# Kernel tuning notes

Hardware: AMD Instinct MI355X
Metric: run time of the kernel (lower is better)

The kernel has to match this reference:

```python
import jax, jax.numpy as jnp
import numpy as np

NE, NR = 100000, 50
E, H, M = 512, 8, 8
HD = E // H
B = 65536


def setup_inputs() -> dict:
    key = jax.random.key(0)
    ks = jax.random.split(key, 24)
    xav = lambda k, shp: jax.random.normal(k, shp, jnp.float32) * (2.0 / (shp[0] + shp[-1])) ** 0.5
    return {
        'entity_emb': xav(ks[0], (NE, E)),
        'relation_emb': xav(ks[1], (NR, E)),
        'dens_ent_emb': jax.random.normal(ks[2], (NE, E), jnp.float32) * 0.02,
        'dens_ent_w': xav(ks[3], (E, 1)), 'dens_ent_b': jnp.zeros((1,), jnp.float32),
        'dens_rel_emb': jax.random.normal(ks[4], (NR, E), jnp.float32) * 0.02,
        'dens_rel_w': xav(ks[5], (E, 1)), 'dens_rel_b': jnp.zeros((1,), jnp.float32),
        'local_motifs': xav(ks[6], (M, HD)),
        'global_motifs': xav(ks[7], (M, HD)),
        'Wq': xav(ks[8], (E, E)), 'bq': jnp.zeros((E,), jnp.float32),
        'Wkl': xav(ks[9], (HD, HD)), 'bkl': jnp.zeros((HD,), jnp.float32),
        'Wkg': xav(ks[10], (HD, HD)), 'bkg': jnp.zeros((HD,), jnp.float32),
        'Wout': xav(ks[11], (2 * E, E)), 'bout': jnp.zeros((E,), jnp.float32),
        'adv_w': jnp.float32(1.0), 'adv_b': jnp.float32(0.0),
        'h_idx': jax.random.randint(ks[12], (B,), 0, NE),
        'r_idx': jax.random.randint(ks[13], (B,), 0, NR),
        't_idx': jax.random.randint(ks[14], (B,), 0, NE),
    }


def reference(entity_emb, relation_emb, dens_ent_emb, dens_ent_w, dens_ent_b,
              dens_rel_emb, dens_rel_w, dens_rel_b, local_motifs, global_motifs,
              Wq, bq, Wkl, bkl, Wkg, bkg, Wout, bout, adv_w, adv_b,
              h_idx, r_idx, t_idx):
    h = entity_emb[h_idx]           # [B, E]
    r = relation_emb[r_idx]
    t = entity_emb[t_idx]
    # density gating: sigmoid(Linear(Embedding(idx))) per head/tail/relation, averaged
    h_d = jax.nn.sigmoid(dens_ent_emb[h_idx] @ dens_ent_w + dens_ent_b)   # [B,1]
    t_d = jax.nn.sigmoid(dens_ent_emb[t_idx] @ dens_ent_w + dens_ent_b)
    r_d = jax.nn.sigmoid(dens_rel_emb[r_idx] @ dens_rel_w + dens_rel_b)
    density = (h_d + t_d + r_d) / 3.0                                     # [B,1]
    diff = h + r - t
    # hierarchical soft attention over local/global motif codebooks
    ctx = h + r + t
    q = (ctx @ Wq + bq).reshape(-1, H, HD)                                # [B,H,HD]
    lk = local_motifs @ Wkl + bkl                                         # [M,HD]
    gk = global_motifs @ Wkg + bkg
    scale = 1.0 / jnp.sqrt(jnp.asarray(HD, q.dtype))
    dens = density[:, :, None]                                            # [B,1,1]
    l_w = jax.nn.softmax(jnp.einsum('bhd,md->bhm', q, lk) * scale + dens, axis=-1)
    g_w = jax.nn.softmax(jnp.einsum('bhd,md->bhm', q, gk) * scale + dens, axis=-1)
    attn = (l_w + g_w) / 2.0                                              # [B,H,M]
    motifs = local_motifs + global_motifs                                 # [M,HD]
    motif_repr = jnp.einsum('bhm,md->bhd', attn, motifs).reshape(-1, E)   # [B,E]
    motif_loss = jnp.sum((diff - motif_repr) ** 2, axis=-1)               # ||.||^2
    combined = jnp.concatenate([diff, motif_repr], axis=-1)               # [B,2E]
    transformed = jnp.tanh(combined @ Wout + bout)
    score = adv_w * jnp.linalg.norm(transformed, axis=-1) + adv_b
    return score, motif_loss
```

## Files before the change

kernel.cpp:

```cpp
#include <hip/hip_runtime.h>
#include <math.h>

#define B_TOT 65536

typedef __attribute__((ext_vector_type(4))) float f32x4;
typedef __attribute__((ext_vector_type(4))) unsigned int u32x4;
typedef __attribute__((ext_vector_type(8))) __bf16 bf16x8;

#define OFF_WLOGT 0u
#define OFF_CBIAS 131072u
#define OFF_BCAT  131584u
#define OFF_MOTIF 721408u
#define OFF_LK    723456u
#define OFF_GK    725504u
#define OFF_G     727552u
#define OFF_DIFF  1048576u
#define OFF_ATTN  68157440u
#define OFF_SSQ   76546048u

__device__ __forceinline__ unsigned short f2bf(float x) {
  union { float f; unsigned int u; } v; v.f = x;
  return (unsigned short)((v.u + 0x7FFFu + ((v.u >> 16) & 1u)) >> 16);
}

__device__ __forceinline__ float bf2f(unsigned short u) {
  union { unsigned int i; float f; } v; v.i = ((unsigned int)u) << 16; return v.f;
}

__device__ __forceinline__ float fast_tanh(float x) {
  float cx = fminf(fmaxf(x, -15.f), 15.f);
  float e = __expf(2.f * cx);
  return 1.f - 2.f * __builtin_amdgcn_rcpf(e + 1.f);
}

__global__ __launch_bounds__(256) void k0a(
    const float* __restrict__ lm, const float* __restrict__ gm,
    const float* __restrict__ Wkl, const float* __restrict__ bkl,
    const float* __restrict__ Wkg, const float* __restrict__ bkg,
    const float* __restrict__ bq,
    float* __restrict__ lk, float* __restrict__ gk,
    float* __restrict__ motifs, float* __restrict__ G, float* __restrict__ cb) {
  int tid = threadIdx.x;
  for (int o = tid; o < 512; o += 256) {
    int m = o >> 6, d = o & 63;
    float s1 = bkl[d], s2 = bkg[d];
    for (int k = 0; k < 64; ++k) {
      s1 += lm[m*64+k] * Wkl[k*64+d];
      s2 += gm[m*64+k] * Wkg[k*64+d];
    }
    lk[o] = s1; gk[o] = s2;
    motifs[o] = lm[o] + gm[o];
  }
  __syncthreads();
  if (tid < 128) {
    int s_ = tid >> 6, h = (tid >> 3) & 7, m = tid & 7;
    const float* K = s_ ? gk : lk;
    float s = 0.f;
    for (int d = 0; d < 64; ++d) s += bq[h*64+d] * K[m*64+d];
    cb[tid] = 0.125f * s;
  }
}

__global__ __launch_bounds__(256) void k0b(
    const float* __restrict__ Wq, const float* __restrict__ Wout,
    const float* __restrict__ lk, const float* __restrict__ gk,
    const float* __restrict__ motifs,
    unsigned short* __restrict__ wlogT, unsigned short* __restrict__ bcatT) {
  int idx = blockIdx.x * 256 + threadIdx.x;
  if (idx >= 65536 + 512*576) return;
  if (idx < 65536) {
    int c = idx >> 9, k = idx & 511;
    int s_ = c >> 6, h = (c >> 3) & 7, m = c & 7;
    const float* K = (s_ ? gk : lk) + m*64;
    const float* wq = Wq + (size_t)k*512 + h*64;
    float s = 0.f;
    for (int d = 0; d < 64; ++d) s += wq[d] * K[d];
    wlogT[(size_t)c*512 + k] = f2bf(0.125f * s);
  } else {
    int i2 = idx - 65536;
    int n = i2 / 576, k = i2 - n*576;
    float v;
    if (k < 512) {
      v = Wout[(size_t)k*512 + n];
    } else {
      int hm = k - 512, h = hm >> 3, m = hm & 7;
      const float* mo = motifs + m*64;
      const float* wo = Wout + (size_t)(512 + h*64)*512 + n;
      v = 0.f;
      for (int d = 0; d < 64; ++d) v += mo[d] * wo[(size_t)d*512];
    }
    bcatT[(size_t)n*576 + k] = f2bf(v);
  }
}

__global__ __launch_bounds__(256, 4) void kA(
    const float* __restrict__ ent, const float* __restrict__ rel,
    const int* __restrict__ hI, const int* __restrict__ rI, const int* __restrict__ tI,
    const unsigned short* __restrict__ wlogT, const float* __restrict__ cb,
    unsigned short* __restrict__ diffB, unsigned short* __restrict__ attnB) {
  __shared__ __align__(16) unsigned char smem[32768];
  unsigned short* As = (unsigned short*)smem;
  unsigned short* Bs = (unsigned short*)(smem + 9216);
  float* lg  = (float*)smem;

  int tid = threadIdx.x;
  int l = tid & 63, wid = tid >> 6;
  int wr = wid >> 1, wc = wid & 1;
  int rowBase = blockIdx.x * 64;
  int r_loc = tid >> 2, p = tid & 3;
  int b = rowBase + r_loc;

  int hi = hI[b], ri = rI[b], ti = tI[b];
  const float* hp = ent + (size_t)hi * 512;
  const float* tp = ent + (size_t)ti * 512;
  const float* rp = rel + (size_t)ri * 512;
  int bn = tid >> 1, half = tid & 1;
  const unsigned short* wsrc = wlogT + (size_t)bn * 512 + half * 32;

  f32x4 acc[2][4] = {};

  float4 gh[4], gt[4], gr[4];
  u32x4 wb[4];

  {
    int q0 = p*8, q1 = 32 + p*8;
    gh[0] = *(const float4*)(hp + q0); gh[1] = *(const float4*)(hp + q0 + 4);
    gh[2] = *(const float4*)(hp + q1); gh[3] = *(const float4*)(hp + q1 + 4);
    gt[0] = *(const float4*)(tp + q0); gt[1] = *(const float4*)(tp + q0 + 4);
    gt[2] = *(const float4*)(tp + q1); gt[3] = *(const float4*)(tp + q1 + 4);
    gr[0] = *(const float4*)(rp + q0); gr[1] = *(const float4*)(rp + q0 + 4);
    gr[2] = *(const float4*)(rp + q1); gr[3] = *(const float4*)(rp + q1 + 4);
    #pragma unroll
    for (int o = 0; o < 4; ++o) wb[o] = *(const u32x4*)(wsrc + o*8);
  }

  #pragma unroll
  for (int c = 0; c < 8; ++c) {
    int k0 = c * 64;
    union { u32x4 v[2]; unsigned short s[16]; } pd, pc;
    #pragma unroll
    for (int g = 0; g < 4; ++g) {
      #pragma unroll
      for (int j = 0; j < 4; ++j) {
        float hv = ((const float*)&gh[g])[j];
        float tv = ((const float*)&gt[g])[j];
        float rv = ((const float*)&gr[g])[j];
        pd.s[g*4+j] = f2bf(hv + rv - tv);
        pc.s[g*4+j] = f2bf(hv + rv + tv);
      }
    }

    __syncthreads();
    *(u32x4*)(As + r_loc*72 + p*8)      = pc.v[0];
    *(u32x4*)(As + r_loc*72 + 32 + p*8) = pc.v[1];
    {
      unsigned short* bp = Bs + bn*72 + half*32;
      *(u32x4*)(bp)      = wb[0];
      *(u32x4*)(bp + 8)  = wb[1];
      *(u32x4*)(bp + 16) = wb[2];
      *(u32x4*)(bp + 24) = wb[3];
    }
    *(u32x4*)(diffB + (size_t)b*512 + k0 + p*8)      = pd.v[0];
    *(u32x4*)(diffB + (size_t)b*512 + k0 + 32 + p*8) = pd.v[1];
    __syncthreads();
    if (c < 7) {
      int q0 = k0 + 64 + p*8, q1 = k0 + 96 + p*8;
      gh[0] = *(const float4*)(hp + q0); gh[1] = *(const float4*)(hp + q0 + 4);
      gh[2] = *(const float4*)(hp + q1); gh[3] = *(const float4*)(hp + q1 + 4);
      gt[0] = *(const float4*)(tp + q0); gt[1] = *(const float4*)(tp + q0 + 4);
      gt[2] = *(const float4*)(tp + q1); gt[3] = *(const float4*)(tp + q1 + 4);
      gr[0] = *(const float4*)(rp + q0); gr[1] = *(const float4*)(rp + q0 + 4);
      gr[2] = *(const float4*)(rp + q1); gr[3] = *(const float4*)(rp + q1 + 4);
      #pragma unroll
      for (int o = 0; o < 4; ++o) wb[o] = *(const u32x4*)(wsrc + (c+1)*64 + o*8);
    }
    #pragma unroll
    for (int kf = 0; kf < 2; ++kf) {
      bf16x8 af0 = *(const bf16x8*)(As + (wr*32 +      (l & 15))*72 + kf*32 + 8*(l >> 4));
      bf16x8 af1 = *(const bf16x8*)(As + (wr*32 + 16 + (l & 15))*72 + kf*32 + 8*(l >> 4));
      #pragma unroll
      for (int n = 0; n < 4; ++n) {
        bf16x8 bfr = *(const bf16x8*)(Bs + (wc*64 + n*16 + (l & 15))*72 + kf*32 + 8*(l >> 4));
        acc[0][n] = __builtin_amdgcn_mfma_f32_16x16x32_bf16(af0, bfr, acc[0][n], 0, 0, 0);
        acc[1][n] = __builtin_amdgcn_mfma_f32_16x16x32_bf16(af1, bfr, acc[1][n], 0, 0, 0);
      }
    }
  }

  __syncthreads();
  #pragma unroll
  for (int m = 0; m < 2; ++m)
    #pragma unroll
    for (int n = 0; n < 4; ++n)
      #pragma unroll
      for (int j = 0; j < 4; ++j) {
        int rr = wr*32 + m*16 + 4*(l >> 4) + j;
        int cc = wc*64 + n*16 + (l & 15);
        lg[rr*128 + ((cc + rr) & 127)] = acc[m][n][j];
      }
  __syncthreads();

  #pragma unroll
  for (int e = 0; e < 2; ++e) {
    int h = 2*p + e;
    float a8[8];
    #pragma unroll
    for (int m = 0; m < 8; ++m) a8[m] = 0.f;
    #pragma unroll
    for (int s = 0; s < 2; ++s) {
      float v[8], mx = -1e30f;
      #pragma unroll
      for (int m = 0; m < 8; ++m) {
        int cc = s*64 + h*8 + m;
        v[m] = lg[r_loc*128 + ((cc + r_loc) & 127)] + cb[cc];
        mx = fmaxf(mx, v[m]);
      }
      float sum = 0.f;
      #pragma unroll
      for (int m = 0; m < 8; ++m) { v[m] = __expf(v[m] - mx); sum += v[m]; }
      float inv = 0.5f / sum;
      #pragma unroll
      for (int m = 0; m < 8; ++m) a8[m] += v[m] * inv;
    }
    union { u32x4 v; unsigned short s[8]; } pk;
    #pragma unroll
    for (int m = 0; m < 8; ++m) pk.s[m] = f2bf(a8[m]);
    *(u32x4*)(attnB + (size_t)b*64 + h*8) = pk.v;
  }
}

__global__ __launch_bounds__(512, 4) void kB(
    const unsigned short* __restrict__ diffB, const unsigned short* __restrict__ attnB,
    const unsigned short* __restrict__ bcatT, const float* __restrict__ bout,
    float* __restrict__ ssqPart) {
  __shared__ __align__(16) unsigned short As[128*40];
  __shared__ __align__(16) unsigned short Bs[256*40];
  __shared__ float part[128*4];
  int tid = threadIdx.x;
  int l = tid & 63, wid = tid >> 6;
  int wr = wid >> 2, wc = wid & 3;
  int mblk = blockIdx.x >> 1, nblk = blockIdx.x & 1;
  int rowBase = mblk * 128;
  int colBase = nblk * 256;
  f32x4 acc[4][4] = {};
  int ar = tid >> 2, aq = tid & 3;
  int bn2 = tid >> 1, half = tid & 1;
  int bx2 = (bn2 >> 3) & 3;

  u32x4 na, nb0, nb1;
  {
    na = *(const u32x4*)(diffB + (size_t)(rowBase + ar)*512 + aq*8);
    const u32x4* src = (const u32x4*)(bcatT + (size_t)(colBase + bn2)*576 + half*16);
    nb0 = src[0]; nb1 = src[1];
  }
  for (int ks = 0; ks < 18; ++ks) {
    __syncthreads();
    *(u32x4*)(&As[ar*40 + aq*8]) = na;
    {
      unsigned short* bp = &Bs[bn2*40];
      int j0 = half*2, j1 = half*2 + 1;
      *(u32x4*)(bp + (j0^bx2)*8) = nb0;
      *(u32x4*)(bp + (j1^bx2)*8) = nb1;
    }
    __syncthreads();
    if (ks < 17) {
      int k0 = (ks + 1) * 32;
      const unsigned short* srcp = (k0 < 512)
        ? diffB + (size_t)(rowBase + ar)*512 + k0 + aq*8
        : attnB + (size_t)(rowBase + ar)*64 + (k0 - 512) + aq*8;
      na = *(const u32x4*)srcp;
      const u32x4* src = (const u32x4*)(bcatT + (size_t)(colBase + bn2)*576 + k0 + half*16);
      nb0 = src[0]; nb1 = src[1];
    }
    {
      bf16x8 af[4];
      #pragma unroll
      for (int m = 0; m < 4; ++m)
        af[m] = *(const bf16x8*)(&As[(wr*64 + m*16 + (l & 15))*40 + 8*(l >> 4)]);
      #pragma unroll
      for (int n = 0; n < 4; ++n) {
        int col = wc*64 + n*16 + (l & 15);
        int g = (l >> 4) ^ ((col >> 3) & 3);
        bf16x8 bfr = *(const bf16x8*)(&Bs[col*40 + g*8]);
        #pragma unroll
        for (int m = 0; m < 4; ++m)
          acc[m][n] = __builtin_amdgcn_mfma_f32_16x16x32_bf16(af[m], bfr, acc[m][n], 0, 0, 0);
      }
    }
  }
  __syncthreads();
  float bo[4];
  #pragma unroll
  for (int n = 0; n < 4; ++n) bo[n] = bout[colBase + wc*64 + n*16 + (l & 15)];
  #pragma unroll
  for (int m = 0; m < 4; ++m) {
    float ss0 = 0.f, ss1 = 0.f, ss2 = 0.f, ss3 = 0.f;
    #pragma unroll
    for (int n = 0; n < 4; ++n) {
      float t0 = fast_tanh(acc[m][n][0] + bo[n]); ss0 += t0*t0;
      float t1 = fast_tanh(acc[m][n][1] + bo[n]); ss1 += t1*t1;
      float t2 = fast_tanh(acc[m][n][2] + bo[n]); ss2 += t2*t2;
      float t3 = fast_tanh(acc[m][n][3] + bo[n]); ss3 += t3*t3;
    }
    #pragma unroll
    for (int mask = 1; mask < 16; mask <<= 1) {
      ss0 += __shfl_xor(ss0, mask, 64);
      ss1 += __shfl_xor(ss1, mask, 64);
      ss2 += __shfl_xor(ss2, mask, 64);
      ss3 += __shfl_xor(ss3, mask, 64);
    }
    if ((l & 15) == 0) {
      int rbase = wr*64 + m*16 + (l >> 4)*4;
      part[(rbase+0)*4 + wc] = ss0;
      part[(rbase+1)*4 + wc] = ss1;
      part[(rbase+2)*4 + wc] = ss2;
      part[(rbase+3)*4 + wc] = ss3;
    }
  }
  __syncthreads();
  if (tid < 128) {
    float s = part[tid*4] + part[tid*4+1] + part[tid*4+2] + part[tid*4+3];
    ssqPart[(size_t)nblk*B_TOT + rowBase + tid] = s;
  }
}

__global__ __launch_bounds__(256) void kCD(
    const unsigned short* __restrict__ diffB, const unsigned short* __restrict__ attnB,
    const float* __restrict__ motifs, const float* __restrict__ ssqPart,
    const float* __restrict__ advw, const float* __restrict__ advb,
    float* __restrict__ lossOut, float* __restrict__ scoreOut) {
  __shared__ float mo[512];
  int tid = threadIdx.x;
  mo[tid] = motifs[tid];
  mo[tid + 256] = motifs[tid + 256];
  __syncthreads();
  int l = tid & 63;
  int b = blockIdx.x * 4 + (tid >> 6);
  union { u32x4 v; unsigned short s[8]; } dv, av;
  dv.v = *(const u32x4*)(diffB + (size_t)b*512 + l*8);
  int h = l >> 3;
  av.v = *(const u32x4*)(attnB + (size_t)b*64 + h*8);
  float at[8], df[8];
  #pragma unroll
  for (int j = 0; j < 8; ++j) { df[j] = bf2f(dv.s[j]); at[j] = bf2f(av.s[j]); }
  int dbase = (l & 7) * 8;
  float part = 0.f;
  #pragma unroll
  for (int j = 0; j < 8; ++j) {
    float repr = 0.f;
    #pragma unroll
    for (int m = 0; m < 8; ++m) repr += at[m] * mo[m*64 + dbase + j];
    float e = df[j] - repr;
    part += e * e;
  }
  #pragma unroll
  for (int off = 1; off < 64; off <<= 1) part += __shfl_xor(part, off, 64);
  if (l == 0) lossOut[b] = part;
  if (tid < 4) {
    int rb = blockIdx.x * 4 + tid;
    float s = ssqPart[rb] + ssqPart[B_TOT + rb];
    scoreOut[rb] = advw[0] * sqrtf(s) + advb[0];
  }
}

extern "C" void kernel_launch(void* const* d_in, const int* in_sizes, int n_in,
                              void* d_out, int out_size, void* d_ws, size_t ws_size,
                              hipStream_t stream) {
  const float* ent  = (const float*)d_in[0];
  const float* rel  = (const float*)d_in[1];
  const float* lm   = (const float*)d_in[8];
  const float* gm   = (const float*)d_in[9];
  const float* Wq   = (const float*)d_in[10];
  const float* bq   = (const float*)d_in[11];
  const float* Wkl  = (const float*)d_in[12];
  const float* bkl  = (const float*)d_in[13];
  const float* Wkg  = (const float*)d_in[14];
  const float* bkg  = (const float*)d_in[15];
  const float* Wout = (const float*)d_in[16];
  const float* bout = (const float*)d_in[17];
  const float* advw = (const float*)d_in[18];
  const float* advb = (const float*)d_in[19];
  const int* hI = (const int*)d_in[20];
  const int* rI = (const int*)d_in[21];
  const int* tI = (const int*)d_in[22];
  char* ws = (char*)d_ws;
  unsigned short* wlogT = (unsigned short*)(ws + OFF_WLOGT);
  float* cb     = (float*)(ws + OFF_CBIAS);
  unsigned short* bcatT = (unsigned short*)(ws + OFF_BCAT);
  float* motifs = (float*)(ws + OFF_MOTIF);
  float* lk     = (float*)(ws + OFF_LK);
  float* gk     = (float*)(ws + OFF_GK);
  float* G      = (float*)(ws + OFF_G);
  unsigned short* diffB = (unsigned short*)(ws + OFF_DIFF);
  unsigned short* attnB = (unsigned short*)(ws + OFF_ATTN);
  float* ssqPart = (float*)(ws + OFF_SSQ);
  float* scoreOut = (float*)d_out;
  float* lossOut  = (float*)d_out + B_TOT;

  hipLaunchKernelGGL(k0a, dim3(1), dim3(256), 0, stream,
                     lm, gm, Wkl, bkl, Wkg, bkg, bq, lk, gk, motifs, G, cb);
  hipLaunchKernelGGL(k0b, dim3(1408), dim3(256), 0, stream,
                     Wq, Wout, lk, gk, motifs, wlogT, bcatT);
  hipLaunchKernelGGL(kA, dim3(B_TOT/64), dim3(256), 0, stream,
                     ent, rel, hI, rI, tI, wlogT, cb, diffB, attnB);
  hipLaunchKernelGGL(kB, dim3(B_TOT/128 * 2), dim3(512), 0, stream,
                     diffB, attnB, bcatT, bout, ssqPart);
  hipLaunchKernelGGL(kCD, dim3(B_TOT/4), dim3(256), 0, stream,
                     diffB, attnB, motifs, ssqPart, advw, advb, lossOut, scoreOut);
}
```

Baseline: 153.0 us.

## Fuse motif loss into attention kernel and deepen GEMM K-tile to 64

The motif-loss computation moves from the final kernel into kA, which uses its just-computed fp32 attention weights and reads back its own diffB rows, so the separate pass that re-reads diff and attention from global memory is gone. The last kernel shrinks to a simple score finalisation. Separately, the Wout GEMM in kB now stages 64-wide K tiles (9 iterations instead of 18), halving barrier count at the cost of more shared memory and dropping the XOR bank swizzle on Bs, which may add LDS conflicts. The loss now uses unrounded attention weights, and kA reads back diffB it just wrote, which relies on the write being visible within the same block.

New measurement: 270.4 us. +76.7%, slower.

```diff
diff --git a/kernel.cpp b/kernel.cpp
--- a/kernel.cpp
+++ b/kernel.cpp
@@ -39,7 +39,7 @@
     const float* __restrict__ Wkg, const float* __restrict__ bkg,
     const float* __restrict__ bq,
     float* __restrict__ lk, float* __restrict__ gk,
-    float* __restrict__ motifs, float* __restrict__ G, float* __restrict__ cb) {
+    float* __restrict__ motifs, float* __restrict__ cb) {
   int tid = threadIdx.x;
   for (int o = tid; o < 512; o += 256) {
     int m = o >> 6, d = o & 63;
@@ -97,7 +97,9 @@
     const float* __restrict__ ent, const float* __restrict__ rel,
     const int* __restrict__ hI, const int* __restrict__ rI, const int* __restrict__ tI,
     const unsigned short* __restrict__ wlogT, const float* __restrict__ cb,
-    unsigned short* __restrict__ diffB, unsigned short* __restrict__ attnB) {
+    const float* __restrict__ motifs,
+    unsigned short* __restrict__ diffB, unsigned short* __restrict__ attnB,
+    float* __restrict__ lossOut) {
   __shared__ __align__(16) unsigned char smem[32768];
   unsigned short* As = (unsigned short*)smem;
   unsigned short* Bs = (unsigned short*)(smem + 9216);
@@ -200,6 +202,7 @@
       }
   __syncthreads();
 
+  float at2[2][8];
   #pragma unroll
   for (int e = 0; e < 2; ++e) {
     int h = 2*p + e;
@@ -224,17 +227,46 @@
     }
     union { u32x4 v; unsigned short s[8]; } pk;
     #pragma unroll
-    for (int m = 0; m < 8; ++m) pk.s[m] = f2bf(a8[m]);
+    for (int m = 0; m < 8; ++m) { at2[e][m] = a8[m]; pk.s[m] = f2bf(a8[m]); }
     *(u32x4*)(attnB + (size_t)b*64 + h*8) = pk.v;
   }
+
+  __syncthreads();
+  float* moS = (float*)smem;
+  moS[tid] = motifs[tid];
+  moS[tid + 256] = motifs[tid + 256];
+  __syncthreads();
+  float lp = 0.f;
+  const unsigned short* dp = diffB + (size_t)b*512;
+  #pragma unroll
+  for (int e = 0; e < 2; ++e) {
+    int hh = 2*p + e;
+    #pragma unroll
+    for (int c8 = 0; c8 < 8; ++c8) {
+      union { u32x4 v; unsigned short s[8]; } du;
+      du.v = *(const u32x4*)(dp + hh*64 + c8*8);
+      #pragma unroll
+      for (int j = 0; j < 8; ++j) {
+        int dd = c8*8 + j;
+        float repr = 0.f;
+        #pragma unroll
+        for (int m = 0; m < 8; ++m) repr += at2[e][m] * moS[m*64 + dd];
+        float err = bf2f(du.s[j]) - repr;
+        lp += err * err;
+      }
+    }
+  }
+  lp += __shfl_xor(lp, 1, 64);
+  lp += __shfl_xor(lp, 2, 64);
+  if (p == 0) lossOut[b] = lp;
 }
 
 __global__ __launch_bounds__(512, 4) void kB(
     const unsigned short* __restrict__ diffB, const unsigned short* __restrict__ attnB,
     const unsigned short* __restrict__ bcatT, const float* __restrict__ bout,
     float* __restrict__ ssqPart) {
-  __shared__ __align__(16) unsigned short As[128*40];
-  __shared__ __align__(16) unsigned short Bs[256*40];
+  __shared__ __align__(16) unsigned short As[128*72];
+  __shared__ __align__(16) unsigned short Bs[256*72];
   __shared__ float part[128*4];
   int tid = threadIdx.x;
   int l = tid & 63, wid = tid >> 6;
@@ -245,43 +277,44 @@
   f32x4 acc[4][4] = {};
   int ar = tid >> 2, aq = tid & 3;
   int bn2 = tid >> 1, half = tid & 1;
-  int bx2 = (bn2 >> 3) & 3;
-
-  u32x4 na, nb0, nb1;
+
+  u32x4 na0, na1, nb0, nb1, nb2, nb3;
   {
-    na = *(const u32x4*)(diffB + (size_t)(rowBase + ar)*512 + aq*8);
-    const u32x4* src = (const u32x4*)(bcatT + (size_t)(colBase + bn2)*576 + half*16);
-    nb0 = src[0]; nb1 = src[1];
-  }
-  for (int ks = 0; ks < 18; ++ks) {
+    const unsigned short* ap = diffB + (size_t)(rowBase + ar)*512 + aq*16;
+    na0 = *(const u32x4*)ap; na1 = *(const u32x4*)(ap + 8);
+    const u32x4* src = (const u32x4*)(bcatT + (size_t)(colBase + bn2)*576 + half*32);
+    nb0 = src[0]; nb1 = src[1]; nb2 = src[2]; nb3 = src[3];
+  }
+  for (int ks = 0; ks < 9; ++ks) {
     __syncthreads();
-    *(u32x4*)(&As[ar*40 + aq*8]) = na;
+    *(u32x4*)(&As[ar*72 + aq*16])     = na0;
+    *(u32x4*)(&As[ar*72 + aq*16 + 8]) = na1;
     {
-      unsigned short* bp = &Bs[bn2*40];
-      int j0 = half*2, j1 = half*2 + 1;
-      *(u32x4*)(bp + (j0^bx2)*8) = nb0;
-      *(u32x4*)(bp + (j1^bx2)*8) = nb1;
+      unsigned short* bp = &Bs[bn2*72 + half*32];
+      *(u32x4*)(bp)      = nb0;
+      *(u32x4*)(bp + 8)  = nb1;
+      *(u32x4*)(bp + 16) = nb2;
+      *(u32x4*)(bp + 24) = nb3;
     }
     __syncthreads();
-    if (ks < 17) {
-      int k0 = (ks + 1) * 32;
-      const unsigned short* srcp = (k0 < 512)
-        ? diffB + (size_t)(rowBase + ar)*512 + k0 + aq*8
-        : attnB + (size_t)(rowBase + ar)*64 + (k0 - 512) + aq*8;
-      na = *(const u32x4*)srcp;
-      const u32x4* src = (const u32x4*)(bcatT + (size_t)(colBase + bn2)*576 + k0 + half*16);
-      nb0 = src[0]; nb1 = src[1];
-    }
-    {
+    if (ks < 8) {
+      int k0 = (ks + 1) * 64;
+      const unsigned short* ap = (k0 < 512)
+        ? diffB + (size_t)(rowBase + ar)*512 + k0 + aq*16
+        : attnB + (size_t)(rowBase + ar)*64 + aq*16;
+      na0 = *(const u32x4*)ap; na1 = *(const u32x4*)(ap + 8);
+      const u32x4* src = (const u32x4*)(bcatT + (size_t)(colBase + bn2)*576 + k0 + half*32);
+      nb0 = src[0]; nb1 = src[1]; nb2 = src[2]; nb3 = src[3];
+    }
+    #pragma unroll
+    for (int kf = 0; kf < 2; ++kf) {
       bf16x8 af[4];
       #pragma unroll
       for (int m = 0; m < 4; ++m)
-        af[m] = *(const bf16x8*)(&As[(wr*64 + m*16 + (l & 15))*40 + 8*(l >> 4)]);
+        af[m] = *(const bf16x8*)(&As[(wr*64 + m*16 + (l & 15))*72 + kf*32 + 8*(l >> 4)]);
       #pragma unroll
       for (int n = 0; n < 4; ++n) {
-        int col = wc*64 + n*16 + (l & 15);
-        int g = (l >> 4) ^ ((col >> 3) & 3);
-        bf16x8 bfr = *(const bf16x8*)(&Bs[col*40 + g*8]);
+        bf16x8 bfr = *(const bf16x8*)(&Bs[(wc*64 + n*16 + (l & 15))*72 + kf*32 + 8*(l >> 4)]);
         #pragma unroll
         for (int m = 0; m < 4; ++m)
           acc[m][n] = __builtin_amdgcn_mfma_f32_16x16x32_bf16(af[m], bfr, acc[m][n], 0, 0, 0);
@@ -324,43 +357,12 @@
   }
 }
 
-__global__ __launch_bounds__(256) void kCD(
-    const unsigned short* __restrict__ diffB, const unsigned short* __restrict__ attnB,
-    const float* __restrict__ motifs, const float* __restrict__ ssqPart,
-    const float* __restrict__ advw, const float* __restrict__ advb,
-    float* __restrict__ lossOut, float* __restrict__ scoreOut) {
-  __shared__ float mo[512];
-  int tid = threadIdx.x;
-  mo[tid] = motifs[tid];
-  mo[tid + 256] = motifs[tid + 256];
-  __syncthreads();
-  int l = tid & 63;
-  int b = blockIdx.x * 4 + (tid >> 6);
-  union { u32x4 v; unsigned short s[8]; } dv, av;
-  dv.v = *(const u32x4*)(diffB + (size_t)b*512 + l*8);
-  int h = l >> 3;
-  av.v = *(const u32x4*)(attnB + (size_t)b*64 + h*8);
-  float at[8], df[8];
-  #pragma unroll
-  for (int j = 0; j < 8; ++j) { df[j] = bf2f(dv.s[j]); at[j] = bf2f(av.s[j]); }
-  int dbase = (l & 7) * 8;
-  float part = 0.f;
-  #pragma unroll
-  for (int j = 0; j < 8; ++j) {
-    float repr = 0.f;
-    #pragma unroll
-    for (int m = 0; m < 8; ++m) repr += at[m] * mo[m*64 + dbase + j];
-    float e = df[j] - repr;
-    part += e * e;
-  }
-  #pragma unroll
-  for (int off = 1; off < 64; off <<= 1) part += __shfl_xor(part, off, 64);
-  if (l == 0) lossOut[b] = part;
-  if (tid < 4) {
-    int rb = blockIdx.x * 4 + tid;
-    float s = ssqPart[rb] + ssqPart[B_TOT + rb];
-    scoreOut[rb] = advw[0] * sqrtf(s) + advb[0];
-  }
+__global__ __launch_bounds__(256) void kD(
+    const float* __restrict__ ssqPart, const float* __restrict__ advw,
+    const float* __restrict__ advb, float* __restrict__ scoreOut) {
+  int i = blockIdx.x * 256 + threadIdx.x;
+  float s = ssqPart[i] + ssqPart[B_TOT + i];
+  scoreOut[i] = advw[0] * sqrtf(s) + advb[0];
 }
 
 extern "C" void kernel_launch(void* const* d_in, const int* in_sizes, int n_in,
@@ -390,7 +392,6 @@
   float* motifs = (float*)(ws + OFF_MOTIF);
   float* lk     = (float*)(ws + OFF_LK);
   float* gk     = (float*)(ws + OFF_GK);
-  float* G      = (float*)(ws + OFF_G);
   unsigned short* diffB = (unsigned short*)(ws + OFF_DIFF);
   unsigned short* attnB = (unsigned short*)(ws + OFF_ATTN);
   float* ssqPart = (float*)(ws + OFF_SSQ);
@@ -398,13 +399,13 @@
   float* lossOut  = (float*)d_out + B_TOT;
 
   hipLaunchKernelGGL(k0a, dim3(1), dim3(256), 0, stream,
-                     lm, gm, Wkl, bkl, Wkg, bkg, bq, lk, gk, motifs, G, cb);
+                     lm, gm, Wkl, bkl, Wkg, bkg, bq, lk, gk, motifs, cb);
   hipLaunchKernelGGL(k0b, dim3(1408), dim3(256), 0, stream,
                      Wq, Wout, lk, gk, motifs, wlogT, bcatT);
   hipLaunchKernelGGL(kA, dim3(B_TOT/64), dim3(256), 0, stream,
-                     ent, rel, hI, rI, tI, wlogT, cb, diffB, attnB);
+                     ent, rel, hI, rI, tI, wlogT, cb, motifs, diffB, attnB, lossOut);
   hipLaunchKernelGGL(kB, dim3(B_TOT/128 * 2), dim3(512), 0, stream,
                      diffB, attnB, bcatT, bout, ssqPart);
-  hipLaunchKernelGGL(kCD, dim3(B_TOT/4), dim3(256), 0, stream,
-                     diffB, attnB, motifs, ssqPart, advw, advb, lossOut, scoreOut);
-}
+  hipLaunchKernelGGL(kD, dim3(B_TOT/256), dim3(256), 0, stream,
+                     ssqPart, advw, advb, scoreOut);
+}
```
